# Performance work log

Measured on AMD Instinct MI355X. Metric: run time of the kernel, lower is better.

The kernel has to match this reference:

```python
import jax, jax.numpy as jnp
import numpy as np

DIM = 20
N = 200000
E = 6400000
ITERATIONS = 3


def setup_inputs() -> dict:
    key = jax.random.key(0)
    ks = jax.random.split(key, 20)
    inp = {
        "h": jax.random.normal(ks[0], (N, DIM), dtype=jnp.float32),
        "node2depth": jax.random.randint(ks[1], (N,), 0, 5, dtype=jnp.int32),
        "edge_src": jax.random.randint(ks[2], (E,), 0, N, dtype=jnp.int32),
        "edge_dst": jax.random.randint(ks[3], (E,), 0, N, dtype=jnp.int32),
    }
    # Six DIM x DIM Linear layers (weight stored [out,in] like torch, plus bias)
    scale = 1.0 / np.sqrt(DIM)
    names = ["Wz", "Uz", "Wr", "Ur", "Wh", "Uh"]
    for j, nm in enumerate(names):
        inp[nm + "_w"] = jax.random.uniform(ks[4 + 2 * j], (DIM, DIM), jnp.float32, -scale, scale)
        inp[nm + "_b"] = jax.random.uniform(ks[5 + 2 * j], (DIM,), jnp.float32, -scale, scale)
    return inp


def _linear(x, w, b):
    return x @ w.T + b


def reference(h, Wz_w, Wz_b, Uz_w, Uz_b, Wr_w, Wr_b, Ur_w, Ur_b,
              Wh_w, Wh_b, Uh_w, Uh_b, node2depth, edge_src, edge_dst):
    active = None
    for i in range(ITERATIONS):
        # active set shrinks as i grows (depth + i <= ITERATIONS)
        active = (node2depth + i) <= ITERATIONS  # [N] bool
        af = active.astype(h.dtype)
        # x[u] = sum over neighbors v of h[v], counting only active src AND active dst
        msg = h[edge_src] * af[edge_src][:, None]          # [E, DIM]
        x = jax.ops.segment_sum(msg, edge_dst, num_segments=N)  # [N, DIM]
        x = x * af[:, None]
        z = jax.nn.sigmoid(_linear(x, Wz_w, Wz_b) + _linear(h, Uz_w, Uz_b))
        r = jax.nn.sigmoid(_linear(x, Wr_w, Wr_b) + _linear(h, Ur_w, Ur_b))
        h_cand = jnp.tanh(_linear(x, Wh_w, Wh_b) + _linear(r * h, Uh_w, Uh_b))
        h_new = z * h + (1.0 - z) * h_cand
        # inactive nodes are dropped from the dict in the original; since the
        # active set only shrinks, keeping their old h is equivalent
        h = jnp.where(active[:, None], h_new, h)
    # original returns only nodes active at the last iteration; zero out the rest
    return jnp.where(active[:, None], h, jnp.zeros_like(h))
```

## Files before the change

kernel.cpp:

```cpp
#include <hip/hip_runtime.h>

#define DIM    20
#define NN     200000
#define EE     6400000
#define ITERS  3
#define BLOCK  256

#define NODES_PER_FINE   64
#define NFINE            3125
#define NCOARSE          98
#define FINE_PER_COARSE  32

#define TILE1            2048
#define IPT1             8

#define TILE             4096
#define IPT              16

#define CAP1             67584
#define NT2P             17
#define CAP2             2304
#define PIPT             9

#define XSTRIDE          21

typedef unsigned int u32;

__device__ __forceinline__ u32 pack_bf16x2(float a, float b) {
    u32 ua = __float_as_uint(a);
    u32 ub = __float_as_uint(b);
    ua = (ua + 0x7FFFu + ((ua >> 16) & 1u)) >> 16;
    ub = (ub + 0x7FFFu + ((ub >> 16) & 1u)) & 0xFFFF0000u;
    return ua | ub;
}

__global__ __launch_bounds__(BLOCK) void setup(const float* __restrict__ h,
                                               const int* __restrict__ depth,
                                               u32* __restrict__ hbA,
                                               u32* __restrict__ hbC,
                                               u32* __restrict__ CT,
                                               int* __restrict__ coarse_cursor,
                                               int* __restrict__ fine_cursor,
                                               int* __restrict__ gcur) {
    int g = blockIdx.x * BLOCK + threadIdx.x;
    if (g < NCOARSE) coarse_cursor[g] = g * CAP1;
    if (g < NFINE)   fine_cursor[g]   = g * CAP2;
    if (g == 0) *gcur = 0;
    if (g < NN / 8) {
        int4 a = *(const int4*)(depth + g * 8);
        int4 b = *(const int4*)(depth + g * 8 + 4);
        CT[g] = ((u32)a.x & 7u)        | (((u32)a.y & 7u) << 4)
              | (((u32)a.z & 7u) << 8) | (((u32)a.w & 7u) << 12)
              | (((u32)b.x & 7u) << 16)| (((u32)b.y & 7u) << 20)
              | (((u32)b.z & 7u) << 24)| (((u32)b.w & 7u) << 28);
    }
    int node = g >> 3, s = g & 7;
    if (depth[node] > ITERS) return;
    float2 f = *(const float2*)(h + (size_t)node * DIM + s * 2);
    hbA[(size_t)node * 8 + s] = pack_bf16x2(f.x, f.y);
    if (s < 2) {
        float2 fc = *(const float2*)(h + (size_t)node * DIM + 16 + s * 2);
        hbC[(size_t)node * 2 + s] = pack_bf16x2(fc.x, fc.y);
    }
}

__global__ __launch_bounds__(BLOCK) void p1_split(const int* __restrict__ esrc,
                                                  const int* __restrict__ edst,
                                                  int* __restrict__ coarse_cursor,
                                                  u32* __restrict__ buf1) {
    __shared__ u32 hist[NCOARSE];
    __shared__ u32 lbase[NCOARSE];
    __shared__ u32 gbase[NCOARSE];
    __shared__ u32 lout[TILE1];
    int tid = threadIdx.x;
    int start = blockIdx.x * TILE1;
    if (tid < NCOARSE) hist[tid] = 0;
    __syncthreads();

    int4 d4[2], s4[2];
    #pragma unroll
    for (int q = 0; q < 2; ++q) {
        int e4 = start + (q * BLOCK + tid) * 4;
        d4[q] = *(const int4*)(edst + e4);
        s4[q] = *(const int4*)(esrc + e4);
    }
    int dd[IPT1], ss[IPT1];
    dd[0]=d4[0].x; dd[1]=d4[0].y; dd[2]=d4[0].z; dd[3]=d4[0].w;
    dd[4]=d4[1].x; dd[5]=d4[1].y; dd[6]=d4[1].z; dd[7]=d4[1].w;
    ss[0]=s4[0].x; ss[1]=s4[0].y; ss[2]=s4[0].z; ss[3]=s4[0].w;
    ss[4]=s4[1].x; ss[5]=s4[1].y; ss[6]=s4[1].z; ss[7]=s4[1].w;

    u32 rank[IPT1];
    #pragma unroll
    for (int k = 0; k < IPT1; ++k)
        rank[k] = atomicAdd(&hist[(u32)dd[k] >> 11], 1u);
    __syncthreads();

    if (tid < 64) {
        u32 a = hist[tid];
        u32 b = (tid + 64 < NCOARSE) ? hist[tid + 64] : 0u;
        u32 ia = a, ib = b;
        #pragma unroll
        for (int off = 1; off < 64; off <<= 1) {
            u32 ta = (u32)__shfl_up((int)ia, off, 64);
            u32 tb = (u32)__shfl_up((int)ib, off, 64);
            if (tid >= off) { ia += ta; ib += tb; }
        }
        u32 totA = (u32)__shfl((int)ia, 63, 64);
        lbase[tid] = ia - a;
        if (tid + 64 < NCOARSE) lbase[tid + 64] = totA + ib - b;
    }
    __syncthreads();
    if (tid < NCOARSE) {
        u32 cq = hist[tid];
        gbase[tid] = cq ? (u32)atomicAdd((u32*)&coarse_cursor[tid], cq) : 0u;
    }
    #pragma unroll
    for (int k = 0; k < IPT1; ++k)
        lout[lbase[(u32)dd[k] >> 11] + rank[k]] = ((u32)dd[k] & 2047u) | ((u32)ss[k] << 11);
    __syncthreads();
    int wid = tid >> 6, lane = tid & 63;
    for (int b = wid; b < NCOARSE; b += 4) {
        u32 cq = hist[b], lb = lbase[b], gb = gbase[b];
        for (u32 i = lane; i < cq; i += 64)
            buf1[gb + i] = lout[lb + i];
    }
}

__global__ __launch_bounds__(BLOCK) void p2_split(const u32* __restrict__ buf1,
                                                  const int* __restrict__ coarse_cursor,
                                                  int* __restrict__ fine_cursor,
                                                  u32* __restrict__ buf2) {
    int bid = blockIdx.x;
    int c = bid / NT2P, t = bid - c * NT2P;
    int base  = c * CAP1;
    int end   = coarse_cursor[c];
    int start = base + t * TILE;
    if (start >= end) return;

    __shared__ u32 hist[FINE_PER_COARSE];
    __shared__ u32 lbase[FINE_PER_COARSE];
    __shared__ u32 gbase[FINE_PER_COARSE];
    __shared__ u32 lout[TILE];
    int tid = threadIdx.x;
    if (tid < FINE_PER_COARSE) hist[tid] = 0;
    __syncthreads();

    u32 w[IPT];
    #pragma unroll
    for (int q = 0; q < 4; ++q) {
        int i4 = start + (q * BLOCK + tid) * 4;
        if (i4 + 3 < end) {
            uint4 v = *(const uint4*)(buf1 + i4);
            w[q * 4 + 0] = v.x; w[q * 4 + 1] = v.y;
            w[q * 4 + 2] = v.z; w[q * 4 + 3] = v.w;
        } else {
            #pragma unroll
            for (int j = 0; j < 4; ++j) {
                int i = i4 + j;
                w[q * 4 + j] = (i < end) ? buf1[i] : 0xFFFFFFFFu;
            }
        }
    }
    u32 rank[IPT];
    #pragma unroll
    for (int k = 0; k < IPT; ++k)
        if (w[k] != 0xFFFFFFFFu)
            rank[k] = atomicAdd(&hist[(w[k] & 2047u) >> 6], 1u);
    __syncthreads();

    if (tid < 32) {
        u32 a = hist[tid], ia = a;
        #pragma unroll
        for (int off = 1; off < 32; off <<= 1) {
            u32 ta = (u32)__shfl_up((int)ia, off, 32);
            if (tid >= off) ia += ta;
        }
        lbase[tid] = ia - a;
        int f = c * FINE_PER_COARSE + tid;
        gbase[tid] = a ? (u32)atomicAdd((u32*)&fine_cursor[f], a) : 0u;
    }
    __syncthreads();
    #pragma unroll
    for (int k = 0; k < IPT; ++k)
        if (w[k] != 0xFFFFFFFFu)
            lout[lbase[(w[k] & 2047u) >> 6] + rank[k]] = (w[k] & 63u) | ((w[k] >> 11) << 6);
    __syncthreads();
    int wid = tid >> 6, lane = tid & 63;
    for (int b = wid; b < FINE_PER_COARSE; b += 4) {
        u32 cq = hist[b], lb = lbase[b], gb = gbase[b];
        for (u32 i = lane; i < cq; i += 64)
            buf2[gb + i] = lout[lb + i];
    }
}


__device__ __forceinline__ float bl(u32 w) { return __uint_as_float(w << 16); }
__device__ __forceinline__ float bh(u32 w) { return __uint_as_float(w & 0xFFFF0000u); }

__device__ __forceinline__ void acc_half(float* xa, float* xc, uint4 a, u32 c) {
    xa[0]+=bl(a.x); xa[1]+=bh(a.x);
    xa[2]+=bl(a.y); xa[3]+=bh(a.y);
    xa[4]+=bl(a.z); xa[5]+=bh(a.z);
    xa[6]+=bl(a.w); xa[7]+=bh(a.w);
    xc[0]+=bl(c);   xc[1]+=bh(c);
}

__device__ __forceinline__ float fast_sigmoid(float t) {
    return 1.0f / (1.0f + __expf(-t));
}
__device__ __forceinline__ float fast_tanh(float t) {
    t = fminf(fmaxf(t, -15.0f), 15.0f);
    float e2 = __expf(2.0f * t);
    return (e2 - 1.0f) / (e2 + 1.0f);
}

__device__ __forceinline__ void gru_body(
    int u, int tid, const float* xl,
    const float* __restrict__ h_in, float* __restrict__ h_out,
    u32* __restrict__ hbA_out, u32* __restrict__ hbC_out,
    int du, int limNext, int isFinal,
    const float* __restrict__ Wz, const float* __restrict__ bWz,
    const float* __restrict__ Uz, const float* __restrict__ bUz,
    const float* __restrict__ Wr, const float* __restrict__ bWr,
    const float* __restrict__ Ur, const float* __restrict__ bUr,
    const float* __restrict__ Wh, const float* __restrict__ bWh,
    const float* __restrict__ Uh, const float* __restrict__ bUh)
{
    float x[DIM], h[DIM];
    #pragma unroll
    for (int k = 0; k < DIM; ++k) x[k] = xl[tid * XSTRIDE + k];
    {
        const float4* hv = (const float4*)(h_in + (size_t)u * DIM);
        float4 a0 = hv[0], a1 = hv[1], a2 = hv[2], a3 = hv[3], a4 = hv[4];
        h[0]=a0.x; h[1]=a0.y; h[2]=a0.z; h[3]=a0.w;
        h[4]=a1.x; h[5]=a1.y; h[6]=a1.z; h[7]=a1.w;
        h[8]=a2.x; h[9]=a2.y; h[10]=a2.z; h[11]=a2.w;
        h[12]=a3.x; h[13]=a3.y; h[14]=a3.z; h[15]=a3.w;
        h[16]=a4.x; h[17]=a4.y; h[18]=a4.z; h[19]=a4.w;
    }

    float z[DIM], rh[DIM];
    #pragma unroll
    for (int j = 0; j < DIM; ++j) {
        float sz = bWz[j] + bUz[j];
        float sr = bWr[j] + bUr[j];
        #pragma unroll
        for (int k = 0; k < DIM; ++k) {
            sz += x[k] * Wz[j * DIM + k];
            sz += h[k] * Uz[j * DIM + k];
            sr += x[k] * Wr[j * DIM + k];
            sr += h[k] * Ur[j * DIM + k];
        }
        z[j]  = fast_sigmoid(sz);
        rh[j] = fast_sigmoid(sr) * h[j];
    }

    float o[DIM];
    #pragma unroll
    for (int j = 0; j < DIM; ++j) {
        float sh = bWh[j] + bUh[j];
        #pragma unroll
        for (int k = 0; k < DIM; ++k) {
            sh += x[k]  * Wh[j * DIM + k];
            sh += rh[k] * Uh[j * DIM + k];
        }
        float hc = fast_tanh(sh);
        o[j] = z[j] * h[j] + (1.0f - z[j]) * hc;
    }

    {
        float4* o4 = (float4*)(h_out + (size_t)u * DIM);
        o4[0] = make_float4(o[0],  o[1],  o[2],  o[3]);
        o4[1] = make_float4(o[4],  o[5],  o[6],  o[7]);
        o4[2] = make_float4(o[8],  o[9],  o[10], o[11]);
        o4[3] = make_float4(o[12], o[13], o[14], o[15]);
        o4[4] = make_float4(o[16], o[17], o[18], o[19]);
    }
    if (!isFinal && du <= limNext) {
        u32* rowA = hbA_out + (size_t)u * 8;
        uint4 wA0 = make_uint4(pack_bf16x2(o[0], o[1]),   pack_bf16x2(o[2], o[3]),
                               pack_bf16x2(o[4], o[5]),   pack_bf16x2(o[6], o[7]));
        uint4 wA1 = make_uint4(pack_bf16x2(o[8], o[9]),   pack_bf16x2(o[10], o[11]),
                               pack_bf16x2(o[12], o[13]), pack_bf16x2(o[14], o[15]));
        *(uint4*)rowA       = wA0;
        *(uint4*)(rowA + 4) = wA1;
        *(uint2*)(hbC_out + (size_t)u * 2) =
            make_uint2(pack_bf16x2(o[16], o[17]), pack_bf16x2(o[18], o[19]));
    }
}

__global__ __launch_bounds__(BLOCK) void pb_gru(
    const u32* __restrict__ buf2, const int* __restrict__ fine_cursor,
    const u32* __restrict__ CT, int* __restrict__ gcur,
    int* __restrict__ ptr, u32* __restrict__ cnt3, u32* __restrict__ ssrc,
    const u32* __restrict__ hbA_in, const u32* __restrict__ hbC_in,
    u32* __restrict__ hbA_out, u32* __restrict__ hbC_out,
    const float* __restrict__ h_in, float* __restrict__ h_out,
    const int* __restrict__ depth,
    const float* __restrict__ Wz, const float* __restrict__ bWz,
    const float* __restrict__ Uz, const float* __restrict__ bUz,
    const float* __restrict__ Wr, const float* __restrict__ bWr,
    const float* __restrict__ Ur, const float* __restrict__ bUr,
    const float* __restrict__ Wh, const float* __restrict__ bWh,
    const float* __restrict__ Uh, const float* __restrict__ bUh)
{
    __shared__ u32 hist[512];
    __shared__ u32 ebase[512];
    __shared__ u32 lout[CAP2];
    __shared__ u32 wsum[4];
    __shared__ int slo;
    __shared__ float xl[64 * XSTRIDE];
    int tid = threadIdx.x;
    int f = blockIdx.x;
    int base = f * CAP2;
    int end  = fine_cursor[f];
    int cnt  = end - base;
    hist[tid] = 0; hist[tid + 256] = 0;
    __syncthreads();

    u32 w[PIPT];
    #pragma unroll
    for (int q = 0; q < 2; ++q) {
        int i4 = base + (q * BLOCK + tid) * 4;
        if (i4 + 3 < end) {
            uint4 v = *(const uint4*)(buf2 + i4);
            w[q * 4 + 0] = v.x; w[q * 4 + 1] = v.y;
            w[q * 4 + 2] = v.z; w[q * 4 + 3] = v.w;
        } else {
            #pragma unroll
            for (int j = 0; j < 4; ++j) {
                int i = i4 + j;
                w[q * 4 + j] = (i < end) ? buf2[i] : 0xFFFFFFFFu;
            }
        }
    }
    {
        int i = base + 2 * BLOCK * 4 + tid;
        w[8] = (i < end) ? buf2[i] : 0xFFFFFFFFu;
    }
    u32 cls[PIPT];
    #pragma unroll
    for (int k = 0; k < PIPT; ++k) {
        u32 s = w[k] >> 6;
        if (s > (u32)(NN - 1)) s = (u32)(NN - 1);
        cls[k] = (CT[s >> 3] >> ((s & 7u) << 2)) & 7u;
    }
    u32 key[PIPT], rank[PIPT];
    #pragma unroll
    for (int k = 0; k < PIPT; ++k) {
        if (w[k] != 0xFFFFFFFFu) {
            key[k]  = (w[k] & 63u) * 8u + cls[k];
            rank[k] = atomicAdd(&hist[key[k]], 1u);
        }
    }
    if (tid == 0) slo = atomicAdd(gcur, cnt);
    __syncthreads();
    {
        u32 s0 = hist[2 * tid], s1 = hist[2 * tid + 1];
        u32 s = s0 + s1;
        int lane = tid & 63, wid = tid >> 6;
        u32 incl = s;
        #pragma unroll
        for (int off = 1; off < 64; off <<= 1) {
            u32 t = __shfl_up((int)incl, off, 64);
            if (lane >= off) incl += t;
        }
        if (lane == 63) wsum[wid] = incl;
        __syncthreads();
        u32 woff = 0;
        for (int w2 = 0; w2 < wid; ++w2) woff += wsum[w2];
        u32 excl = woff + incl - s;
        ebase[2 * tid]     = excl;
        ebase[2 * tid + 1] = excl + s0;
    }
    __syncthreads();
    int lo = slo;
    if (tid < NODES_PER_FINE) {
        u32 base0 = ebase[tid * 8];
        u32 cc1 = ebase[tid * 8 + 2] - base0;
        u32 cc2 = ebase[tid * 8 + 3] - base0;
        u32 cc3 = ebase[tid * 8 + 4] - base0;
        int u = f * NODES_PER_FINE + tid;
        ptr[u]  = lo + (int)base0;
        cnt3[u] = cc1 | (cc2 << 10) | (cc3 << 20);
    }
    #pragma unroll
    for (int k = 0; k < PIPT; ++k) {
        if (w[k] != 0xFFFFFFFFu) lout[ebase[key[k]] + rank[k]] = w[k] >> 6;
    }
    __syncthreads();
    for (int j = tid; j < cnt; j += BLOCK) ssrc[lo + j] = lout[j];

    int t = tid & 7, team = tid >> 3;
    int r = t >> 1, q = t & 1;
    #pragma unroll
    for (int rep = 0; rep < 2; ++rep) {
        int nl = team + rep * 32;
        int u = f * NODES_PER_FINE + nl;
        if (depth[u] <= ITERS) {
            int b0 = (int)ebase[nl * 8];
            int d  = (int)(ebase[nl * 8 + 4] - ebase[nl * 8]);

            float xa[8], xc[2];
            #pragma unroll
            for (int k = 0; k < 8; ++k) xa[k] = 0.0f;
            xc[0] = 0.0f; xc[1] = 0.0f;

            int e = r;
            for (; e + 12 < d; e += 16) {
                u32 p0 = lout[b0 + e];
                u32 p1 = lout[b0 + e + 4];
                u32 p2 = lout[b0 + e + 8];
                u32 p3 = lout[b0 + e + 12];
                uint4 a0 = *(const uint4*)(hbA_in + (size_t)p0 * 8 + q * 4);
                uint4 a1 = *(const uint4*)(hbA_in + (size_t)p1 * 8 + q * 4);
                uint4 a2 = *(const uint4*)(hbA_in + (size_t)p2 * 8 + q * 4);
                uint4 a3 = *(const uint4*)(hbA_in + (size_t)p3 * 8 + q * 4);
                u32 c0 = hbC_in[(size_t)p0 * 2 + q];
                u32 c1 = hbC_in[(size_t)p1 * 2 + q];
                u32 c2 = hbC_in[(size_t)p2 * 2 + q];
                u32 c3 = hbC_in[(size_t)p3 * 2 + q];
                acc_half(xa, xc, a0, c0);
                acc_half(xa, xc, a1, c1);
                acc_half(xa, xc, a2, c2);
                acc_half(xa, xc, a3, c3);
            }
            for (; e + 4 < d; e += 8) {
                u32 p0 = lout[b0 + e];
                u32 p1 = lout[b0 + e + 4];
                uint4 a0 = *(const uint4*)(hbA_in + (size_t)p0 * 8 + q * 4);
                uint4 a1 = *(const uint4*)(hbA_in + (size_t)p1 * 8 + q * 4);
                u32 c0 = hbC_in[(size_t)p0 * 2 + q];
                u32 c1 = hbC_in[(size_t)p1 * 2 + q];
                acc_half(xa, xc, a0, c0);
                acc_half(xa, xc, a1, c1);
            }
            if (e < d) {
                u32 p0 = lout[b0 + e];
                uint4 a0 = *(const uint4*)(hbA_in + (size_t)p0 * 8 + q * 4);
                u32 c0 = hbC_in[(size_t)p0 * 2 + q];
                acc_half(xa, xc, a0, c0);
            }
            #pragma unroll
            for (int k = 0; k < 8; ++k) {
                xa[k] += __shfl_xor(xa[k], 2, 64);
                xa[k] += __shfl_xor(xa[k], 4, 64);
            }
            xc[0] += __shfl_xor(xc[0], 2, 64); xc[0] += __shfl_xor(xc[0], 4, 64);
            xc[1] += __shfl_xor(xc[1], 2, 64); xc[1] += __shfl_xor(xc[1], 4, 64);

            float* xr = xl + nl * XSTRIDE;
            if (t == 0) {
                #pragma unroll
                for (int k = 0; k < 8; ++k) xr[k] = xa[k];
                xr[16] = xc[0]; xr[17] = xc[1];
            } else if (t == 1) {
                #pragma unroll
                for (int k = 0; k < 8; ++k) xr[8 + k] = xa[k];
                xr[18] = xc[0]; xr[19] = xc[1];
            }
        }
    }
    __syncthreads();
    if (tid >= 64) return;

    int u = f * NODES_PER_FINE + tid;
    int du = depth[u];
    if (du > ITERS) return;
    gru_body(u, tid, xl, h_in, h_out, hbA_out, hbC_out, du, 2, 0,
             Wz, bWz, Uz, bUz, Wr, bWr, Ur, bUr, Wh, bWh, Uh, bUh);
}


__global__ __launch_bounds__(BLOCK) void grnn_iter(
    const u32* __restrict__ hbA_in, const u32* __restrict__ hbC_in,
    u32* __restrict__ hbA_out, u32* __restrict__ hbC_out,
    const float* __restrict__ h_in, float* __restrict__ h_out,
    const int* __restrict__ depth, const int* __restrict__ ptr,
    const u32* __restrict__ cnt3, const u32* __restrict__ ssrc,
    const float* __restrict__ Wz, const float* __restrict__ bWz,
    const float* __restrict__ Uz, const float* __restrict__ bUz,
    const float* __restrict__ Wr, const float* __restrict__ bWr,
    const float* __restrict__ Ur, const float* __restrict__ bUr,
    const float* __restrict__ Wh, const float* __restrict__ bWh,
    const float* __restrict__ Uh, const float* __restrict__ bUh,
    int lim, int limNext, int shift, int isFinal)
{
    __shared__ float xl[64 * XSTRIDE];
    int tid = threadIdx.x;
    int t = tid & 7, team = tid >> 3;
    int r = t >> 1, q = t & 1;

    #pragma unroll
    for (int rep = 0; rep < 2; ++rep) {
        int nl = team + rep * 32;
        int u = blockIdx.x * 64 + nl;
        if (depth[u] <= lim) {
            int p = ptr[u];
            int d = (int)((cnt3[u] >> shift) & 1023u);

            float xa[8], xc[2];
            #pragma unroll
            for (int k = 0; k < 8; ++k) xa[k] = 0.0f;
            xc[0] = 0.0f; xc[1] = 0.0f;

            int e = r;
            for (; e + 12 < d; e += 16) {
                u32 p0 = ssrc[p + e];
                u32 p1 = ssrc[p + e + 4];
                u32 p2 = ssrc[p + e + 8];
                u32 p3 = ssrc[p + e + 12];
                uint4 a0 = *(const uint4*)(hbA_in + (size_t)p0 * 8 + q * 4);
                uint4 a1 = *(const uint4*)(hbA_in + (size_t)p1 * 8 + q * 4);
                uint4 a2 = *(const uint4*)(hbA_in + (size_t)p2 * 8 + q * 4);
                uint4 a3 = *(const uint4*)(hbA_in + (size_t)p3 * 8 + q * 4);
                u32 c0 = hbC_in[(size_t)p0 * 2 + q];
                u32 c1 = hbC_in[(size_t)p1 * 2 + q];
                u32 c2 = hbC_in[(size_t)p2 * 2 + q];
                u32 c3 = hbC_in[(size_t)p3 * 2 + q];
                acc_half(xa, xc, a0, c0);
                acc_half(xa, xc, a1, c1);
                acc_half(xa, xc, a2, c2);
                acc_half(xa, xc, a3, c3);
            }
            for (; e + 4 < d; e += 8) {
                u32 p0 = ssrc[p + e];
                u32 p1 = ssrc[p + e + 4];
                uint4 a0 = *(const uint4*)(hbA_in + (size_t)p0 * 8 + q * 4);
                uint4 a1 = *(const uint4*)(hbA_in + (size_t)p1 * 8 + q * 4);
                u32 c0 = hbC_in[(size_t)p0 * 2 + q];
                u32 c1 = hbC_in[(size_t)p1 * 2 + q];
                acc_half(xa, xc, a0, c0);
                acc_half(xa, xc, a1, c1);
            }
            if (e < d) {
                u32 p0 = ssrc[p + e];
                uint4 a0 = *(const uint4*)(hbA_in + (size_t)p0 * 8 + q * 4);
                u32 c0 = hbC_in[(size_t)p0 * 2 + q];
                acc_half(xa, xc, a0, c0);
            }
            #pragma unroll
            for (int k = 0; k < 8; ++k) {
                xa[k] += __shfl_xor(xa[k], 2, 64);
                xa[k] += __shfl_xor(xa[k], 4, 64);
            }
            xc[0] += __shfl_xor(xc[0], 2, 64); xc[0] += __shfl_xor(xc[0], 4, 64);
            xc[1] += __shfl_xor(xc[1], 2, 64); xc[1] += __shfl_xor(xc[1], 4, 64);

            float* xr = xl + nl * XSTRIDE;
            if (t == 0) {
                #pragma unroll
                for (int k = 0; k < 8; ++k) xr[k] = xa[k];
                xr[16] = xc[0]; xr[17] = xc[1];
            } else if (t == 1) {
                #pragma unroll
                for (int k = 0; k < 8; ++k) xr[8 + k] = xa[k];
                xr[18] = xc[0]; xr[19] = xc[1];
            }
        }
    }
    __syncthreads();
    if (tid >= 64) return;

    int u = blockIdx.x * 64 + tid;
    int du = depth[u];
    if (du > lim) {
        if (isFinal) {
            float4 z4 = make_float4(0.f, 0.f, 0.f, 0.f);
            float4* o4 = (float4*)(h_out + (size_t)u * DIM);
            #pragma unroll
            for (int qq = 0; qq < 5; ++qq) o4[qq] = z4;
        }
        return;
    }
    gru_body(u, tid, xl, h_in, h_out, hbA_out, hbC_out, du, limNext, isFinal,
             Wz, bWz, Uz, bUz, Wr, bWr, Ur, bUr, Wh, bWh, Uh, bUh);
}


extern "C" void kernel_launch(void* const* d_in, const int* in_sizes, int n_in,
                              void* d_out, int out_size, void* d_ws, size_t ws_size,
                              hipStream_t stream) {
    const float* h0    = (const float*)d_in[0];
    const int*   depth = (const int*)d_in[1];
    const int*   esrc  = (const int*)d_in[2];
    const int*   edst  = (const int*)d_in[3];
    const float* Wz  = (const float*)d_in[4];  const float* bWz = (const float*)d_in[5];
    const float* Uz  = (const float*)d_in[6];  const float* bUz = (const float*)d_in[7];
    const float* Wr  = (const float*)d_in[8];  const float* bWr = (const float*)d_in[9];
    const float* Ur  = (const float*)d_in[10]; const float* bUr = (const float*)d_in[11];
    const float* Wh  = (const float*)d_in[12]; const float* bWh = (const float*)d_in[13];
    const float* Uh  = (const float*)d_in[14]; const float* bUh = (const float*)d_in[15];
    float* out = (float*)d_out;

    int* W = (int*)d_ws;
    u32*  CT            = (u32*)(W + 0);
    int*  gcur          = W + 25024;
    int*  coarse_cursor = W + 25088;
    int*  fine_cursor   = W + 25216;
    int*  ptr           = W + 28416;
    u32*  cnt3          = (u32*)(W + 228416);
    u32*  buf1          = (u32*)(W + 428416);
    u32*  buf2          = buf1 + (size_t)NCOARSE * CAP1;
    float* h1           = (float*)(buf2 + (size_t)NFINE * CAP2);
    u32*  hbA0          = (u32*)(h1 + (size_t)NN * DIM);
    u32*  hbC0          = hbA0 + (size_t)NN * 8;
    u32*  hbA1          = hbC0 + (size_t)NN * 2;
    u32*  hbC1          = hbA1 + (size_t)NN * 8;
    u32*  ssrc          = buf1;

    setup   <<<(NN * 8) / BLOCK, BLOCK, 0, stream>>>(h0, depth, hbA0, hbC0, CT,
                                                     coarse_cursor, fine_cursor, gcur);
    p1_split<<<EE / TILE1, BLOCK, 0, stream>>>(esrc, edst, coarse_cursor, buf1);
    p2_split<<<NCOARSE * NT2P, BLOCK, 0, stream>>>(buf1, coarse_cursor, fine_cursor, buf2);

    pb_gru  <<<NFINE, BLOCK, 0, stream>>>(buf2, fine_cursor, CT, gcur, ptr, cnt3, ssrc,
        hbA0, hbC0, hbA1, hbC1, h0, h1, depth,
        Wz, bWz, Uz, bUz, Wr, bWr, Ur, bUr, Wh, bWh, Uh, bUh);

    grnn_iter<<<NN / 64, BLOCK, 0, stream>>>(hbA1, hbC1, hbA0, hbC0, h1, h1,
        depth, ptr, cnt3, ssrc,
        Wz, bWz, Uz, bUz, Wr, bWr, Ur, bUr, Wh, bWh, Uh, bUh, 2, 1, 10, 0);
    grnn_iter<<<NN / 64, BLOCK, 0, stream>>>(hbA0, hbC0, hbA1, hbC1, h1, out,
        depth, ptr, cnt3, ssrc,
        Wz, bWz, Uz, bUz, Wr, bWr, Ur, bUr, Wh, bWh, Uh, bUh, 1, 0, 0, 1);
}
```

Baseline: 489.4 us.

## Renumber source nodes by depth and drop inactive-source edges early

Adds a counting sort of nodes by depth (histogram, scan, scatter kernels) that yields a permutation. Packed bf16 hidden states are stored in permuted order, so each source's activity class is a comparison against cumulative boundaries instead of a packed depth-table lookup. Edges whose source is inactive (depth 4) are filtered out in the first partition pass, which shrinks buffers and downstream work, and the bucket capacities are reduced to match. The cost is three extra small kernels plus a random perm gather per edge in p1_split, and the smaller capacities assume the filtered edge counts fit.

```diff
diff --git a/kernel.cpp b/kernel.cpp
--- a/kernel.cpp
+++ b/kernel.cpp
@@ -17,14 +17,75 @@
 #define TILE             4096
 #define IPT              16
 
-#define CAP1             67584
-#define NT2P             17
-#define CAP2             2304
-#define PIPT             9
+#define CAP1             57344
+#define NT2P             14
+#define CAP2             2048
+#define PIPT             8
 
 #define XSTRIDE          21
 
 typedef unsigned int u32;
+
+__global__ __launch_bounds__(BLOCK) void kdep(const int* __restrict__ depth,
+                                              int* __restrict__ dcnt) {
+    __shared__ u32 dh[5];
+    int tid = threadIdx.x;
+    if (tid < 5) dh[tid] = 0;
+    __syncthreads();
+    for (int n = blockIdx.x * BLOCK + tid; n < NN; n += gridDim.x * BLOCK)
+        atomicAdd(&dh[depth[n]], 1u);
+    __syncthreads();
+    if (tid < 5) dcnt[tid * 256 + blockIdx.x] = (int)dh[tid];
+}
+
+__global__ __launch_bounds__(BLOCK) void k2_scan(const int* __restrict__ dcnt,
+                                                 int* __restrict__ dbase,
+                                                 int* __restrict__ cum) {
+    __shared__ int wsum[4];
+    __shared__ int sdb[1281];
+    int tid = threadIdx.x;
+    int lane = tid & 63, wid = tid >> 6;
+    const int CH2 = 5;
+    int loc[CH2];
+    int base = tid * CH2;
+    int s = 0;
+    #pragma unroll
+    for (int j = 0; j < CH2; ++j) { int v = dcnt[base + j]; loc[j] = v; s += v; }
+    int incl = s;
+    #pragma unroll
+    for (int off = 1; off < 64; off <<= 1) {
+        int t = __shfl_up(incl, off, 64);
+        if (lane >= off) incl += t;
+    }
+    if (lane == 63) wsum[wid] = incl;
+    __syncthreads();
+    int woff = 0;
+    for (int w = 0; w < wid; ++w) woff += wsum[w];
+    int run = woff + incl - s;
+    #pragma unroll
+    for (int j = 0; j < CH2; ++j) {
+        sdb[base + j]   = run;
+        dbase[base + j] = run;
+        run += loc[j];
+    }
+    if (tid == 255) sdb[1280] = run;
+    __syncthreads();
+    if (tid < 5) cum[tid] = sdb[(tid + 1) * 256];
+}
+
+__global__ __launch_bounds__(BLOCK) void kd_scatter(const int* __restrict__ depth,
+                                                    const int* __restrict__ dbase,
+                                                    int* __restrict__ perm) {
+    __shared__ u32 dh[5];
+    int tid = threadIdx.x;
+    if (tid < 5) dh[tid] = 0;
+    __syncthreads();
+    for (int n = blockIdx.x * BLOCK + tid; n < NN; n += gridDim.x * BLOCK) {
+        int d = depth[n];
+        u32 r = atomicAdd(&dh[d], 1u);
+        perm[n] = dbase[d * 256 + blockIdx.x] + (int)r;
+    }
+}
 
 __device__ __forceinline__ u32 pack_bf16x2(float a, float b) {
     u32 ua = __float_as_uint(a);
@@ -36,9 +97,9 @@
 
 __global__ __launch_bounds__(BLOCK) void setup(const float* __restrict__ h,
                                                const int* __restrict__ depth,
+                                               const int* __restrict__ perm,
                                                u32* __restrict__ hbA,
                                                u32* __restrict__ hbC,
-                                               u32* __restrict__ CT,
                                                int* __restrict__ coarse_cursor,
                                                int* __restrict__ fine_cursor,
                                                int* __restrict__ gcur) {
@@ -46,26 +107,21 @@
     if (g < NCOARSE) coarse_cursor[g] = g * CAP1;
     if (g < NFINE)   fine_cursor[g]   = g * CAP2;
     if (g == 0) *gcur = 0;
-    if (g < NN / 8) {
-        int4 a = *(const int4*)(depth + g * 8);
-        int4 b = *(const int4*)(depth + g * 8 + 4);
-        CT[g] = ((u32)a.x & 7u)        | (((u32)a.y & 7u) << 4)
-              | (((u32)a.z & 7u) << 8) | (((u32)a.w & 7u) << 12)
-              | (((u32)b.x & 7u) << 16)| (((u32)b.y & 7u) << 20)
-              | (((u32)b.z & 7u) << 24)| (((u32)b.w & 7u) << 28);
-    }
     int node = g >> 3, s = g & 7;
     if (depth[node] > ITERS) return;
+    int pid = perm[node];
     float2 f = *(const float2*)(h + (size_t)node * DIM + s * 2);
-    hbA[(size_t)node * 8 + s] = pack_bf16x2(f.x, f.y);
+    hbA[(size_t)pid * 8 + s] = pack_bf16x2(f.x, f.y);
     if (s < 2) {
         float2 fc = *(const float2*)(h + (size_t)node * DIM + 16 + s * 2);
-        hbC[(size_t)node * 2 + s] = pack_bf16x2(fc.x, fc.y);
+        hbC[(size_t)pid * 2 + s] = pack_bf16x2(fc.x, fc.y);
     }
 }
 
 __global__ __launch_bounds__(BLOCK) void p1_split(const int* __restrict__ esrc,
                                                   const int* __restrict__ edst,
+                                                  const int* __restrict__ perm,
+                                                  const int* __restrict__ cum,
                                                   int* __restrict__ coarse_cursor,
                                                   u32* __restrict__ buf1) {
     __shared__ u32 hist[NCOARSE];
@@ -76,6 +132,7 @@
     int start = blockIdx.x * TILE1;
     if (tid < NCOARSE) hist[tid] = 0;
     __syncthreads();
+    const u32 c3 = (u32)cum[3];
 
     int4 d4[2], s4[2];
     #pragma unroll
@@ -84,16 +141,21 @@
         d4[q] = *(const int4*)(edst + e4);
         s4[q] = *(const int4*)(esrc + e4);
     }
-    int dd[IPT1], ss[IPT1];
+    u32 pid[IPT1];
+    pid[0] = (u32)perm[s4[0].x]; pid[1] = (u32)perm[s4[0].y];
+    pid[2] = (u32)perm[s4[0].z]; pid[3] = (u32)perm[s4[0].w];
+    pid[4] = (u32)perm[s4[1].x]; pid[5] = (u32)perm[s4[1].y];
+    pid[6] = (u32)perm[s4[1].z]; pid[7] = (u32)perm[s4[1].w];
+    asm volatile("" :: "v"(pid[0]), "v"(pid[1]), "v"(pid[2]), "v"(pid[3]),
+                       "v"(pid[4]), "v"(pid[5]), "v"(pid[6]), "v"(pid[7]));
+    int dd[IPT1];
     dd[0]=d4[0].x; dd[1]=d4[0].y; dd[2]=d4[0].z; dd[3]=d4[0].w;
     dd[4]=d4[1].x; dd[5]=d4[1].y; dd[6]=d4[1].z; dd[7]=d4[1].w;
-    ss[0]=s4[0].x; ss[1]=s4[0].y; ss[2]=s4[0].z; ss[3]=s4[0].w;
-    ss[4]=s4[1].x; ss[5]=s4[1].y; ss[6]=s4[1].z; ss[7]=s4[1].w;
 
     u32 rank[IPT1];
     #pragma unroll
     for (int k = 0; k < IPT1; ++k)
-        rank[k] = atomicAdd(&hist[(u32)dd[k] >> 11], 1u);
+        if (pid[k] < c3) rank[k] = atomicAdd(&hist[(u32)dd[k] >> 11], 1u);
     __syncthreads();
 
     if (tid < 64) {
@@ -117,7 +179,8 @@
     }
     #pragma unroll
     for (int k = 0; k < IPT1; ++k)
-        lout[lbase[(u32)dd[k] >> 11] + rank[k]] = ((u32)dd[k] & 2047u) | ((u32)ss[k] << 11);
+        if (pid[k] < c3)
+            lout[lbase[(u32)dd[k] >> 11] + rank[k]] = ((u32)dd[k] & 2047u) | (pid[k] << 11);
     __syncthreads();
     int wid = tid >> 6, lane = tid & 63;
     for (int b = wid; b < NCOARSE; b += 4) {
@@ -216,10 +279,10 @@
 }
 
 __device__ __forceinline__ void gru_body(
-    int u, int tid, const float* xl,
+    int u, int pid, int tid, const float* xl,
     const float* __restrict__ h_in, float* __restrict__ h_out,
     u32* __restrict__ hbA_out, u32* __restrict__ hbC_out,
-    int du, int limNext, int isFinal,
+    int cumNext, int isFinal,
     const float* __restrict__ Wz, const float* __restrict__ bWz,
     const float* __restrict__ Uz, const float* __restrict__ bUz,
     const float* __restrict__ Wr, const float* __restrict__ bWr,
@@ -277,27 +340,27 @@
         o4[3] = make_float4(o[12], o[13], o[14], o[15]);
         o4[4] = make_float4(o[16], o[17], o[18], o[19]);
     }
-    if (!isFinal && du <= limNext) {
-        u32* rowA = hbA_out + (size_t)u * 8;
+    if (!isFinal && pid < cumNext) {
+        u32* rowA = hbA_out + (size_t)pid * 8;
         uint4 wA0 = make_uint4(pack_bf16x2(o[0], o[1]),   pack_bf16x2(o[2], o[3]),
                                pack_bf16x2(o[4], o[5]),   pack_bf16x2(o[6], o[7]));
         uint4 wA1 = make_uint4(pack_bf16x2(o[8], o[9]),   pack_bf16x2(o[10], o[11]),
                                pack_bf16x2(o[12], o[13]), pack_bf16x2(o[14], o[15]));
         *(uint4*)rowA       = wA0;
         *(uint4*)(rowA + 4) = wA1;
-        *(uint2*)(hbC_out + (size_t)u * 2) =
+        *(uint2*)(hbC_out + (size_t)pid * 2) =
             make_uint2(pack_bf16x2(o[16], o[17]), pack_bf16x2(o[18], o[19]));
     }
 }
 
 __global__ __launch_bounds__(BLOCK) void pb_gru(
     const u32* __restrict__ buf2, const int* __restrict__ fine_cursor,
-    const u32* __restrict__ CT, int* __restrict__ gcur,
+    const int* __restrict__ cum, int* __restrict__ gcur,
     int* __restrict__ ptr, u32* __restrict__ cnt3, u32* __restrict__ ssrc,
     const u32* __restrict__ hbA_in, const u32* __restrict__ hbC_in,
     u32* __restrict__ hbA_out, u32* __restrict__ hbC_out,
     const float* __restrict__ h_in, float* __restrict__ h_out,
-    const int* __restrict__ depth,
+    const int* __restrict__ depth, const int* __restrict__ perm,
     const float* __restrict__ Wz, const float* __restrict__ bWz,
     const float* __restrict__ Uz, const float* __restrict__ bUz,
     const float* __restrict__ Wr, const float* __restrict__ bWr,
@@ -316,6 +379,7 @@
     int base = f * CAP2;
     int end  = fine_cursor[f];
     int cnt  = end - base;
+    u32 c0 = (u32)cum[0], c1 = (u32)cum[1], c2 = (u32)cum[2];
     hist[tid] = 0; hist[tid + 256] = 0;
     __syncthreads();
 
@@ -335,22 +399,13 @@
             }
         }
     }
-    {
-        int i = base + 2 * BLOCK * 4 + tid;
-        w[8] = (i < end) ? buf2[i] : 0xFFFFFFFFu;
-    }
-    u32 cls[PIPT];
-    #pragma unroll
-    for (int k = 0; k < PIPT; ++k) {
-        u32 s = w[k] >> 6;
-        if (s > (u32)(NN - 1)) s = (u32)(NN - 1);
-        cls[k] = (CT[s >> 3] >> ((s & 7u) << 2)) & 7u;
-    }
     u32 key[PIPT], rank[PIPT];
     #pragma unroll
     for (int k = 0; k < PIPT; ++k) {
         if (w[k] != 0xFFFFFFFFu) {
-            key[k]  = (w[k] & 63u) * 8u + cls[k];
+            u32 pid = w[k] >> 6;
+            u32 cls = (u32)(pid >= c0) + (u32)(pid >= c1) + (u32)(pid >= c2);
+            key[k]  = (w[k] & 63u) * 8u + cls;
             rank[k] = atomicAdd(&hist[key[k]], 1u);
         }
     }
@@ -417,30 +472,30 @@
                 uint4 a1 = *(const uint4*)(hbA_in + (size_t)p1 * 8 + q * 4);
                 uint4 a2 = *(const uint4*)(hbA_in + (size_t)p2 * 8 + q * 4);
                 uint4 a3 = *(const uint4*)(hbA_in + (size_t)p3 * 8 + q * 4);
-                u32 c0 = hbC_in[(size_t)p0 * 2 + q];
-                u32 c1 = hbC_in[(size_t)p1 * 2 + q];
-                u32 c2 = hbC_in[(size_t)p2 * 2 + q];
-                u32 c3 = hbC_in[(size_t)p3 * 2 + q];
-                acc_half(xa, xc, a0, c0);
-                acc_half(xa, xc, a1, c1);
-                acc_half(xa, xc, a2, c2);
-                acc_half(xa, xc, a3, c3);
+                u32 cc0 = hbC_in[(size_t)p0 * 2 + q];
+                u32 cc1 = hbC_in[(size_t)p1 * 2 + q];
+                u32 cc2 = hbC_in[(size_t)p2 * 2 + q];
+                u32 cc3 = hbC_in[(size_t)p3 * 2 + q];
+                acc_half(xa, xc, a0, cc0);
+                acc_half(xa, xc, a1, cc1);
+                acc_half(xa, xc, a2, cc2);
+                acc_half(xa, xc, a3, cc3);
             }
             for (; e + 4 < d; e += 8) {
                 u32 p0 = lout[b0 + e];
                 u32 p1 = lout[b0 + e + 4];
                 uint4 a0 = *(const uint4*)(hbA_in + (size_t)p0 * 8 + q * 4);
                 uint4 a1 = *(const uint4*)(hbA_in + (size_t)p1 * 8 + q * 4);
-                u32 c0 = hbC_in[(size_t)p0 * 2 + q];
-                u32 c1 = hbC_in[(size_t)p1 * 2 + q];
-                acc_half(xa, xc, a0, c0);
-                acc_half(xa, xc, a1, c1);
+                u32 cc0 = hbC_in[(size_t)p0 * 2 + q];
+                u32 cc1 = hbC_in[(size_t)p1 * 2 + q];
+                acc_half(xa, xc, a0, cc0);
+                acc_half(xa, xc, a1, cc1);
             }
             if (e < d) {
                 u32 p0 = lout[b0 + e];
                 uint4 a0 = *(const uint4*)(hbA_in + (size_t)p0 * 8 + q * 4);
-                u32 c0 = hbC_in[(size_t)p0 * 2 + q];
-                acc_half(xa, xc, a0, c0);
+                u32 cc0 = hbC_in[(size_t)p0 * 2 + q];
+                acc_half(xa, xc, a0, cc0);
             }
             #pragma unroll
             for (int k = 0; k < 8; ++k) {
@@ -466,9 +521,9 @@
     if (tid >= 64) return;
 
     int u = f * NODES_PER_FINE + tid;
-    int du = depth[u];
-    if (du > ITERS) return;
-    gru_body(u, tid, xl, h_in, h_out, hbA_out, hbC_out, du, 2, 0,
+    if (depth[u] > ITERS) return;
+    int pid = perm[u];
+    gru_body(u, pid, tid, xl, h_in, h_out, hbA_out, hbC_out, (int)c2, 0,
              Wz, bWz, Uz, bUz, Wr, bWr, Ur, bUr, Wh, bWh, Uh, bUh);
 }
 
@@ -477,15 +532,17 @@
     const u32* __restrict__ hbA_in, const u32* __restrict__ hbC_in,
     u32* __restrict__ hbA_out, u32* __restrict__ hbC_out,
     const float* __restrict__ h_in, float* __restrict__ h_out,
-    const int* __restrict__ depth, const int* __restrict__ ptr,
-    const u32* __restrict__ cnt3, const u32* __restrict__ ssrc,
+    const int* __restrict__ depth, const int* __restrict__ perm,
+    const int* __restrict__ cum,
+    const int* __restrict__ ptr, const u32* __restrict__ cnt3,
+    const u32* __restrict__ ssrc,
     const float* __restrict__ Wz, const float* __restrict__ bWz,
     const float* __restrict__ Uz, const float* __restrict__ bUz,
     const float* __restrict__ Wr, const float* __restrict__ bWr,
     const float* __restrict__ Ur, const float* __restrict__ bUr,
     const float* __restrict__ Wh, const float* __restrict__ bWh,
     const float* __restrict__ Uh, const float* __restrict__ bUh,
-    int lim, int limNext, int shift, int isFinal)
+    int lim, int cumIdx, int shift, int isFinal)
 {
     __shared__ float xl[64 * XSTRIDE];
     int tid = threadIdx.x;
@@ -515,30 +572,30 @@
                 uint4 a1 = *(const uint4*)(hbA_in + (size_t)p1 * 8 + q * 4);
                 uint4 a2 = *(const uint4*)(hbA_in + (size_t)p2 * 8 + q * 4);
                 uint4 a3 = *(const uint4*)(hbA_in + (size_t)p3 * 8 + q * 4);
-                u32 c0 = hbC_in[(size_t)p0 * 2 + q];
-                u32 c1 = hbC_in[(size_t)p1 * 2 + q];
-                u32 c2 = hbC_in[(size_t)p2 * 2 + q];
-                u32 c3 = hbC_in[(size_t)p3 * 2 + q];
-                acc_half(xa, xc, a0, c0);
-                acc_half(xa, xc, a1, c1);
-                acc_half(xa, xc, a2, c2);
-                acc_half(xa, xc, a3, c3);
+                u32 cc0 = hbC_in[(size_t)p0 * 2 + q];
+                u32 cc1 = hbC_in[(size_t)p1 * 2 + q];
+                u32 cc2 = hbC_in[(size_t)p2 * 2 + q];
+                u32 cc3 = hbC_in[(size_t)p3 * 2 + q];
+                acc_half(xa, xc, a0, cc0);
+                acc_half(xa, xc, a1, cc1);
+                acc_half(xa, xc, a2, cc2);
+                acc_half(xa, xc, a3, cc3);
             }
             for (; e + 4 < d; e += 8) {
                 u32 p0 = ssrc[p + e];
                 u32 p1 = ssrc[p + e + 4];
                 uint4 a0 = *(const uint4*)(hbA_in + (size_t)p0 * 8 + q * 4);
                 uint4 a1 = *(const uint4*)(hbA_in + (size_t)p1 * 8 + q * 4);
-                u32 c0 = hbC_in[(size_t)p0 * 2 + q];
-                u32 c1 = hbC_in[(size_t)p1 * 2 + q];
-                acc_half(xa, xc, a0, c0);
-                acc_half(xa, xc, a1, c1);
+                u32 cc0 = hbC_in[(size_t)p0 * 2 + q];
+                u32 cc1 = hbC_in[(size_t)p1 * 2 + q];
+                acc_half(xa, xc, a0, cc0);
+                acc_half(xa, xc, a1, cc1);
             }
             if (e < d) {
                 u32 p0 = ssrc[p + e];
                 uint4 a0 = *(const uint4*)(hbA_in + (size_t)p0 * 8 + q * 4);
-                u32 c0 = hbC_in[(size_t)p0 * 2 + q];
-                acc_half(xa, xc, a0, c0);
+                u32 cc0 = hbC_in[(size_t)p0 * 2 + q];
+                acc_half(xa, xc, a0, cc0);
             }
             #pragma unroll
             for (int k = 0; k < 8; ++k) {
@@ -564,8 +621,7 @@
     if (tid >= 64) return;
 
     int u = blockIdx.x * 64 + tid;
-    int du = depth[u];
-    if (du > lim) {
+    if (depth[u] > lim) {
         if (isFinal) {
             float4 z4 = make_float4(0.f, 0.f, 0.f, 0.f);
             float4* o4 = (float4*)(h_out + (size_t)u * DIM);
@@ -574,7 +630,8 @@
         }
         return;
     }
-    gru_body(u, tid, xl, h_in, h_out, hbA_out, hbC_out, du, limNext, isFinal,
+    int pid = perm[u];
+    gru_body(u, pid, tid, xl, h_in, h_out, hbA_out, hbC_out, cum[cumIdx], isFinal,
              Wz, bWz, Uz, bUz, Wr, bWr, Ur, bUr, Wh, bWh, Uh, bUh);
 }
 
@@ -595,13 +652,16 @@
     float* out = (float*)d_out;
 
     int* W = (int*)d_ws;
-    u32*  CT            = (u32*)(W + 0);
-    int*  gcur          = W + 25024;
-    int*  coarse_cursor = W + 25088;
-    int*  fine_cursor   = W + 25216;
-    int*  ptr           = W + 28416;
-    u32*  cnt3          = (u32*)(W + 228416);
-    u32*  buf1          = (u32*)(W + 428416);
+    int*  dcnt          = W + 0;
+    int*  dbase         = W + 1280;
+    int*  cum           = W + 2560;
+    int*  gcur          = W + 2568;
+    int*  coarse_cursor = W + 2576;
+    int*  fine_cursor   = W + 2688;
+    int*  ptr           = W + 5824;
+    u32*  cnt3          = (u32*)(W + 205824);
+    int*  perm          = W + 405824;
+    u32*  buf1          = (u32*)(W + 605824);
     u32*  buf2          = buf1 + (size_t)NCOARSE * CAP1;
     float* h1           = (float*)(buf2 + (size_t)NFINE * CAP2);
     u32*  hbA0          = (u32*)(h1 + (size_t)NN * DIM);
@@ -610,19 +670,22 @@
     u32*  hbC1          = hbA1 + (size_t)NN * 8;
     u32*  ssrc          = buf1;
 
-    setup   <<<(NN * 8) / BLOCK, BLOCK, 0, stream>>>(h0, depth, hbA0, hbC0, CT,
-                                                     coarse_cursor, fine_cursor, gcur);
-    p1_split<<<EE / TILE1, BLOCK, 0, stream>>>(esrc, edst, coarse_cursor, buf1);
-    p2_split<<<NCOARSE * NT2P, BLOCK, 0, stream>>>(buf1, coarse_cursor, fine_cursor, buf2);
-
-    pb_gru  <<<NFINE, BLOCK, 0, stream>>>(buf2, fine_cursor, CT, gcur, ptr, cnt3, ssrc,
-        hbA0, hbC0, hbA1, hbC1, h0, h1, depth,
+    kdep      <<<256, BLOCK, 0, stream>>>(depth, dcnt);
+    k2_scan   <<<1,   BLOCK, 0, stream>>>(dcnt, dbase, cum);
+    kd_scatter<<<256, BLOCK, 0, stream>>>(depth, dbase, perm);
+    setup     <<<(NN * 8) / BLOCK, BLOCK, 0, stream>>>(h0, depth, perm, hbA0, hbC0,
+                                                       coarse_cursor, fine_cursor, gcur);
+    p1_split  <<<EE / TILE1, BLOCK, 0, stream>>>(esrc, edst, perm, cum, coarse_cursor, buf1);
+    p2_split  <<<NCOARSE * NT2P, BLOCK, 0, stream>>>(buf1, coarse_cursor, fine_cursor, buf2);
+
+    pb_gru    <<<NFINE, BLOCK, 0, stream>>>(buf2, fine_cursor, cum, gcur, ptr, cnt3, ssrc,
+        hbA0, hbC0, hbA1, hbC1, h0, h1, depth, perm,
         Wz, bWz, Uz, bUz, Wr, bWr, Ur, bUr, Wh, bWh, Uh, bUh);
 
     grnn_iter<<<NN / 64, BLOCK, 0, stream>>>(hbA1, hbC1, hbA0, hbC0, h1, h1,
-        depth, ptr, cnt3, ssrc,
+        depth, perm, cum, ptr, cnt3, ssrc,
         Wz, bWz, Uz, bUz, Wr, bWr, Ur, bUr, Wh, bWh, Uh, bUh, 2, 1, 10, 0);
     grnn_iter<<<NN / 64, BLOCK, 0, stream>>>(hbA0, hbC0, hbA1, hbC1, h1, out,
-        depth, ptr, cnt3, ssrc,
+        depth, perm, cum, ptr, cnt3, ssrc,
         Wz, bWz, Uz, bUz, Wr, bWr, Ur, bUr, Wh, bWh, Uh, bUh, 1, 0, 0, 1);
 }
```

New measurement: 603.7 us. 1.23x slower.

## Filter inactive-source edges at first partition pass and carry depth class in key

Applied to the files above, without the earlier changes.

The first partition pass now looks up each edge's source depth class from the packed class table and drops edges whose source is never active (class above 3). The class is encoded in the upper bits of the packed word, so the fused GRU kernel no longer does its own table lookup. Fewer edges pass through, so the buffer capacities, tile counts and per-thread item counts are reduced. The risk is that the smaller fixed capacities could overflow if the filtered edge counts per bucket exceed them.

```diff
diff --git a/kernel.cpp b/kernel.cpp
--- a/kernel.cpp
+++ b/kernel.cpp
@@ -17,10 +17,10 @@
 #define TILE             4096
 #define IPT              16
 
-#define CAP1             67584
-#define NT2P             17
-#define CAP2             2304
-#define PIPT             9
+#define CAP1             57344
+#define NT2P             14
+#define CAP2             2048
+#define PIPT             8
 
 #define XSTRIDE          21
 
@@ -66,6 +66,7 @@
 
 __global__ __launch_bounds__(BLOCK) void p1_split(const int* __restrict__ esrc,
                                                   const int* __restrict__ edst,
+                                                  const u32* __restrict__ CT,
                                                   int* __restrict__ coarse_cursor,
                                                   u32* __restrict__ buf1) {
     __shared__ u32 hist[NCOARSE];
@@ -90,10 +91,17 @@
     ss[0]=s4[0].x; ss[1]=s4[0].y; ss[2]=s4[0].z; ss[3]=s4[0].w;
     ss[4]=s4[1].x; ss[5]=s4[1].y; ss[6]=s4[1].z; ss[7]=s4[1].w;
 
+    u32 cls[IPT1];
+    #pragma unroll
+    for (int k = 0; k < IPT1; ++k)
+        cls[k] = (CT[(u32)ss[k] >> 3] >> (((u32)ss[k] & 7u) << 2)) & 7u;
+    asm volatile("" :: "v"(cls[0]), "v"(cls[1]), "v"(cls[2]), "v"(cls[3]),
+                       "v"(cls[4]), "v"(cls[5]), "v"(cls[6]), "v"(cls[7]));
+
     u32 rank[IPT1];
     #pragma unroll
     for (int k = 0; k < IPT1; ++k)
-        rank[k] = atomicAdd(&hist[(u32)dd[k] >> 11], 1u);
+        if (cls[k] <= 3u) rank[k] = atomicAdd(&hist[(u32)dd[k] >> 11], 1u);
     __syncthreads();
 
     if (tid < 64) {
@@ -117,7 +125,9 @@
     }
     #pragma unroll
     for (int k = 0; k < IPT1; ++k)
-        lout[lbase[(u32)dd[k] >> 11] + rank[k]] = ((u32)dd[k] & 2047u) | ((u32)ss[k] << 11);
+        if (cls[k] <= 3u)
+            lout[lbase[(u32)dd[k] >> 11] + rank[k]] =
+                ((u32)dd[k] & 2047u) | ((u32)ss[k] << 11) | (cls[k] << 29);
     __syncthreads();
     int wid = tid >> 6, lane = tid & 63;
     for (int b = wid; b < NCOARSE; b += 4) {
@@ -292,7 +302,7 @@
 
 __global__ __launch_bounds__(BLOCK) void pb_gru(
     const u32* __restrict__ buf2, const int* __restrict__ fine_cursor,
-    const u32* __restrict__ CT, int* __restrict__ gcur,
+    int* __restrict__ gcur,
     int* __restrict__ ptr, u32* __restrict__ cnt3, u32* __restrict__ ssrc,
     const u32* __restrict__ hbA_in, const u32* __restrict__ hbC_in,
     u32* __restrict__ hbA_out, u32* __restrict__ hbC_out,
@@ -335,22 +345,12 @@
             }
         }
     }
-    {
-        int i = base + 2 * BLOCK * 4 + tid;
-        w[8] = (i < end) ? buf2[i] : 0xFFFFFFFFu;
-    }
-    u32 cls[PIPT];
-    #pragma unroll
-    for (int k = 0; k < PIPT; ++k) {
-        u32 s = w[k] >> 6;
-        if (s > (u32)(NN - 1)) s = (u32)(NN - 1);
-        cls[k] = (CT[s >> 3] >> ((s & 7u) << 2)) & 7u;
-    }
     u32 key[PIPT], rank[PIPT];
     #pragma unroll
     for (int k = 0; k < PIPT; ++k) {
         if (w[k] != 0xFFFFFFFFu) {
-            key[k]  = (w[k] & 63u) * 8u + cls[k];
+            u32 cls = (w[k] >> 24) & 7u;
+            key[k]  = (w[k] & 63u) * 8u + cls;
             rank[k] = atomicAdd(&hist[key[k]], 1u);
         }
     }
@@ -387,7 +387,7 @@
     }
     #pragma unroll
     for (int k = 0; k < PIPT; ++k) {
-        if (w[k] != 0xFFFFFFFFu) lout[ebase[key[k]] + rank[k]] = w[k] >> 6;
+        if (w[k] != 0xFFFFFFFFu) lout[ebase[key[k]] + rank[k]] = (w[k] >> 6) & 0x3FFFFu;
     }
     __syncthreads();
     for (int j = tid; j < cnt; j += BLOCK) ssrc[lo + j] = lout[j];
@@ -417,30 +417,30 @@
                 uint4 a1 = *(const uint4*)(hbA_in + (size_t)p1 * 8 + q * 4);
                 uint4 a2 = *(const uint4*)(hbA_in + (size_t)p2 * 8 + q * 4);
                 uint4 a3 = *(const uint4*)(hbA_in + (size_t)p3 * 8 + q * 4);
-                u32 c0 = hbC_in[(size_t)p0 * 2 + q];
-                u32 c1 = hbC_in[(size_t)p1 * 2 + q];
-                u32 c2 = hbC_in[(size_t)p2 * 2 + q];
-                u32 c3 = hbC_in[(size_t)p3 * 2 + q];
-                acc_half(xa, xc, a0, c0);
-                acc_half(xa, xc, a1, c1);
-                acc_half(xa, xc, a2, c2);
-                acc_half(xa, xc, a3, c3);
+                u32 cc0 = hbC_in[(size_t)p0 * 2 + q];
+                u32 cc1 = hbC_in[(size_t)p1 * 2 + q];
+                u32 cc2 = hbC_in[(size_t)p2 * 2 + q];
+                u32 cc3 = hbC_in[(size_t)p3 * 2 + q];
+                acc_half(xa, xc, a0, cc0);
+                acc_half(xa, xc, a1, cc1);
+                acc_half(xa, xc, a2, cc2);
+                acc_half(xa, xc, a3, cc3);
             }
             for (; e + 4 < d; e += 8) {
                 u32 p0 = lout[b0 + e];
                 u32 p1 = lout[b0 + e + 4];
                 uint4 a0 = *(const uint4*)(hbA_in + (size_t)p0 * 8 + q * 4);
                 uint4 a1 = *(const uint4*)(hbA_in + (size_t)p1 * 8 + q * 4);
-                u32 c0 = hbC_in[(size_t)p0 * 2 + q];
-                u32 c1 = hbC_in[(size_t)p1 * 2 + q];
-                acc_half(xa, xc, a0, c0);
-                acc_half(xa, xc, a1, c1);
+                u32 cc0 = hbC_in[(size_t)p0 * 2 + q];
+                u32 cc1 = hbC_in[(size_t)p1 * 2 + q];
+                acc_half(xa, xc, a0, cc0);
+                acc_half(xa, xc, a1, cc1);
             }
             if (e < d) {
                 u32 p0 = lout[b0 + e];
                 uint4 a0 = *(const uint4*)(hbA_in + (size_t)p0 * 8 + q * 4);
-                u32 c0 = hbC_in[(size_t)p0 * 2 + q];
-                acc_half(xa, xc, a0, c0);
+                u32 cc0 = hbC_in[(size_t)p0 * 2 + q];
+                acc_half(xa, xc, a0, cc0);
             }
             #pragma unroll
             for (int k = 0; k < 8; ++k) {
@@ -515,30 +515,30 @@
                 uint4 a1 = *(const uint4*)(hbA_in + (size_t)p1 * 8 + q * 4);
                 uint4 a2 = *(const uint4*)(hbA_in + (size_t)p2 * 8 + q * 4);
                 uint4 a3 = *(const uint4*)(hbA_in + (size_t)p3 * 8 + q * 4);
-                u32 c0 = hbC_in[(size_t)p0 * 2 + q];
-                u32 c1 = hbC_in[(size_t)p1 * 2 + q];
-                u32 c2 = hbC_in[(size_t)p2 * 2 + q];
-                u32 c3 = hbC_in[(size_t)p3 * 2 + q];
-                acc_half(xa, xc, a0, c0);
-                acc_half(xa, xc, a1, c1);
-                acc_half(xa, xc, a2, c2);
-                acc_half(xa, xc, a3, c3);
+                u32 cc0 = hbC_in[(size_t)p0 * 2 + q];
+                u32 cc1 = hbC_in[(size_t)p1 * 2 + q];
+                u32 cc2 = hbC_in[(size_t)p2 * 2 + q];
+                u32 cc3 = hbC_in[(size_t)p3 * 2 + q];
+                acc_half(xa, xc, a0, cc0);
+                acc_half(xa, xc, a1, cc1);
+                acc_half(xa, xc, a2, cc2);
+                acc_half(xa, xc, a3, cc3);
             }
             for (; e + 4 < d; e += 8) {
                 u32 p0 = ssrc[p + e];
                 u32 p1 = ssrc[p + e + 4];
                 uint4 a0 = *(const uint4*)(hbA_in + (size_t)p0 * 8 + q * 4);
                 uint4 a1 = *(const uint4*)(hbA_in + (size_t)p1 * 8 + q * 4);
-                u32 c0 = hbC_in[(size_t)p0 * 2 + q];
-                u32 c1 = hbC_in[(size_t)p1 * 2 + q];
-                acc_half(xa, xc, a0, c0);
-                acc_half(xa, xc, a1, c1);
+                u32 cc0 = hbC_in[(size_t)p0 * 2 + q];
+                u32 cc1 = hbC_in[(size_t)p1 * 2 + q];
+                acc_half(xa, xc, a0, cc0);
+                acc_half(xa, xc, a1, cc1);
             }
             if (e < d) {
                 u32 p0 = ssrc[p + e];
                 uint4 a0 = *(const uint4*)(hbA_in + (size_t)p0 * 8 + q * 4);
-                u32 c0 = hbC_in[(size_t)p0 * 2 + q];
-                acc_half(xa, xc, a0, c0);
+                u32 cc0 = hbC_in[(size_t)p0 * 2 + q];
+                acc_half(xa, xc, a0, cc0);
             }
             #pragma unroll
             for (int k = 0; k < 8; ++k) {
@@ -612,10 +612,10 @@
 
     setup   <<<(NN * 8) / BLOCK, BLOCK, 0, stream>>>(h0, depth, hbA0, hbC0, CT,
                                                      coarse_cursor, fine_cursor, gcur);
-    p1_split<<<EE / TILE1, BLOCK, 0, stream>>>(esrc, edst, coarse_cursor, buf1);
+    p1_split<<<EE / TILE1, BLOCK, 0, stream>>>(esrc, edst, CT, coarse_cursor, buf1);
     p2_split<<<NCOARSE * NT2P, BLOCK, 0, stream>>>(buf1, coarse_cursor, fine_cursor, buf2);
 
-    pb_gru  <<<NFINE, BLOCK, 0, stream>>>(buf2, fine_cursor, CT, gcur, ptr, cnt3, ssrc,
+    pb_gru  <<<NFINE, BLOCK, 0, stream>>>(buf2, fine_cursor, gcur, ptr, cnt3, ssrc,
         hbA0, hbC0, hbA1, hbC1, h0, h1, depth,
         Wz, bWz, Uz, bUz, Wr, bWr, Ur, bUr, Wh, bWh, Uh, bUh);
 
```

After: 485.1 us (median of 2 runs). Within noise of the previous version (-0.9%).
